# Optimization experiments

Hardware: AMD Instinct MI355X
Metric: run time of the kernel (lower is better)

Reference implementation:

```python
import jax, jax.numpy as jnp
import numpy as np

N = 100000   # nodes
E = 1600000  # edges
IN, H1, H2, OUT = 512, 64, 16, 40


def setup_inputs() -> dict:
    key = jax.random.key(0)
    ks = jax.random.split(key, 8)
    x = jax.random.normal(ks[0], (N, IN), jnp.float32)
    edge_index = jax.random.randint(ks[1], (2, E), 0, N, dtype=jnp.int64)

    def glorot(k, i, o):
        s = np.sqrt(6.0 / (i + o)).astype(np.float32)
        return jax.random.uniform(k, (i, o), jnp.float32, -s, s)

    return dict(
        x=x, edge_index=edge_index,
        W1=glorot(ks[2], IN, H1), b1=jnp.zeros((H1,), jnp.float32),
        W2=glorot(ks[3], H1, H2), b2=jnp.zeros((H2,), jnp.float32),
        W3=glorot(ks[4], H2, OUT), b3=jnp.zeros((OUT,), jnp.float32),
    )


def _gcn_conv(x, src, dst, W, b):
    # PyG GCNConv: x' = D^{-1/2} (A + I) D^{-1/2} (x W) + b
    h = x @ W                                   # [N, F_out]
    n = x.shape[0]
    deg = jnp.zeros((n,), h.dtype).at[dst].add(1.0) + 1.0   # self-loop adds 1
    dinv = jax.lax.rsqrt(deg)                   # deg >= 1 always
    norm = dinv[src] * dinv[dst]                # [E]
    msg = h[src] * norm[:, None]                # gather + scale  [E, F_out]
    out = jnp.zeros_like(h).at[dst].add(msg)    # scatter-add to targets
    out = out + h * (dinv * dinv)[:, None]      # self-loop contribution
    return out + b


def reference(x, edge_index, W1, b1, W2, b2, W3, b3):
    src, dst = edge_index[0], edge_index[1]
    h = jax.nn.relu(_gcn_conv(x, src, dst, W1, b1))
    # dropout(p=0.2, training=False) -> identity
    h = jax.nn.relu(_gcn_conv(h, src, dst, W2, b2))
    h = _gcn_conv(h, src, dst, W3, b3)
    return jax.nn.log_softmax(h, axis=-1)
```

## Files before the change

### kernel.cpp

```cpp
#include <hip/hip_runtime.h>
#include <cstdint>
#include <cstddef>

#define NNODES 100000
#define NEDGES 1600000
#define NWIN 100
#define WIN_NODES 1000
#define WCAP 17408
#define WSTR 16

#define GM_ROWS 64
#define GEMM_BLOCKS ((NNODES + GM_ROWS - 1) / GM_ROWS)
#define BUCKET_BLOCKS 512
#define BCHUNK ((NEDGES + BUCKET_BLOCKS - 1) / BUCKET_BLOCKS)
#define MEGA_BLOCKS (GEMM_BLOCKS + BUCKET_BLOCKS)

typedef __attribute__((ext_vector_type(8))) short bf16x8;
typedef __attribute__((ext_vector_type(4))) float f32x4;

__device__ inline unsigned short f2bf(float f) {
    union { float f; unsigned u; } v; v.f = f;
    unsigned r = v.u + 0x7FFFu + ((v.u >> 16) & 1u);
    return (unsigned short)(r >> 16);
}
__device__ inline void bfpair(unsigned u, float& lo, float& hi) {
    union { unsigned x; float f; } a, b;
    a.x = u << 16; b.x = u & 0xffff0000u;
    lo = a.f; hi = b.f;
}

#define GLOAD_LDS16(gp, lp)                                                        \
    __builtin_amdgcn_global_load_lds(                                              \
        (__attribute__((address_space(1))) const void*)(gp),                       \
        (__attribute__((address_space(3))) void*)(lp), 16, 0, 0)


__global__ __launch_bounds__(256) void convW(const float* __restrict__ W,
                                             unsigned short* __restrict__ Wt,
                                             int* __restrict__ wcur) {
    if (blockIdx.x == 0 && threadIdx.x < NWIN) wcur[threadIdx.x * WSTR] = 0;
    int i = blockIdx.x * 256 + threadIdx.x;
    if (i < 512 * 64) {
        int k = i >> 6, n = i & 63;
        Wt[n * 512 + k] = f2bf(W[i]);
    }
}


__global__ __launch_bounds__(256) void mega_gemm_bucket(
        const float* __restrict__ A,
        const unsigned short* __restrict__ Wt,
        unsigned short* __restrict__ Hs,
        const int* __restrict__ src, const int* __restrict__ dst,
        unsigned* __restrict__ stage,
        int* __restrict__ wcur, int M, int E) {
    __shared__ __align__(16) char smem[32768];

    long long b = blockIdx.x;
    int g0 = (int)((b * GEMM_BLOCKS) / MEGA_BLOCKS);
    int g1 = (int)(((b + 1) * GEMM_BLOCKS) / MEGA_BLOCKS);

    if (g1 > g0) {
        const int tid = threadIdx.x;
        const int wv = tid >> 6;
        const int lane = tid & 63;
        const int lm = lane & 15;
        const int lk8 = (lane >> 4);
        const int bm = g0 * GM_ROWS;
        const int wbase = bm + wv * 16;

        f32x4 acc[4];
#pragma unroll
        for (int j = 0; j < 4; j++) acc[j] = (f32x4){0.f, 0.f, 0.f, 0.f};

        const int st_rl = lane >> 4;
        const int st_u = lane & 15;

        auto ISSUE_A = [&](int k0, int bsel) {
#pragma unroll
            for (int i = 0; i < 4; i++) {
                int rl = 4 * i + st_rl;
                int grow = wbase + rl;
                grow = min(grow, M - 1);
                int su = st_u ^ rl;
                const float* gp = A + (size_t)grow * 512 + k0 + su * 4;
                char* lp = smem + bsel * 16384 + wv * 4096 + i * 1024;
                GLOAD_LDS16(gp, lp);
            }
        };

        ISSUE_A(0, 0);
        for (int t = 0; t < 8; t++) {
            const int k0 = t * 64;
            const int bsel = t & 1;

            bf16x8 bb[4][2];
#pragma unroll
            for (int cf = 0; cf < 4; cf++)
#pragma unroll
                for (int kf = 0; kf < 2; kf++)
                    bb[cf][kf] = *(const bf16x8*)&Wt[(size_t)(cf * 16 + lm) * 512
                                                     + k0 + kf * 32 + lk8 * 8];

            if (t < 7) ISSUE_A(k0 + 64, bsel ^ 1);

            if (t < 7) { asm volatile("s_waitcnt vmcnt(4)" ::: "memory"); }
            else       { asm volatile("s_waitcnt vmcnt(0)" ::: "memory"); }
            __builtin_amdgcn_sched_barrier(0);

            bf16x8 af[2];
#pragma unroll
            for (int kf = 0; kf < 2; kf++) {
                int u0 = kf * 8 + (lk8 << 1);
                const char* base = smem + bsel * 16384 + wv * 4096 + lm * 256;
                float4 lo = *(const float4*)(base + (((u0)     ^ lm) << 4));
                float4 hi = *(const float4*)(base + (((u0 + 1) ^ lm) << 4));
                unsigned c[4];
                asm("v_cvt_pk_bf16_f32 %0, %1, %2" : "=v"(c[0]) : "v"(lo.x), "v"(lo.y));
                asm("v_cvt_pk_bf16_f32 %0, %1, %2" : "=v"(c[1]) : "v"(lo.z), "v"(lo.w));
                asm("v_cvt_pk_bf16_f32 %0, %1, %2" : "=v"(c[2]) : "v"(hi.x), "v"(hi.y));
                asm("v_cvt_pk_bf16_f32 %0, %1, %2" : "=v"(c[3]) : "v"(hi.z), "v"(hi.w));
                af[kf] = *(bf16x8*)c;
            }

            __builtin_amdgcn_s_setprio(1);
#pragma unroll
            for (int kf = 0; kf < 2; kf++)
#pragma unroll
                for (int cf = 0; cf < 4; cf++)
                    acc[cf] = __builtin_amdgcn_mfma_f32_16x16x32_bf16(
                        af[kf], bb[cf][kf], acc[cf], 0, 0, 0);
            __builtin_amdgcn_s_setprio(0);
        }

#pragma unroll
        for (int j = 0; j < 4; j++) {
            int row = wbase + (lane >> 4) * 4 + j;
            if (row < M) {
#pragma unroll
                for (int cf = 0; cf < 4; cf++)
                    Hs[(size_t)row * 64 + cf * 16 + lm] = f2bf(acc[cf][j]);
            }
        }
    } else {
        int bi = (int)(b - g0);
        int* cnt  = (int*)smem;
        int* lcur = cnt + NWIN;
        const int tid = threadIdx.x;
        int e0 = bi * BCHUNK;
        int e1 = e0 + BCHUNK; if (e1 > E) e1 = E;

        for (int i = tid; i < NWIN; i += 256) cnt[i] = 0;
        __syncthreads();
        for (int e = e0 + tid; e < e1; e += 256)
            atomicAdd(&cnt[dst[e] / WIN_NODES], 1);
        __syncthreads();
        for (int i = tid; i < NWIN; i += 256)
            lcur[i] = atomicAdd(&wcur[i * WSTR], cnt[i]);
        __syncthreads();
        for (int e = e0 + tid; e < e1; e += 256) {
            int d = dst[e], s = src[e];
            int w = d / WIN_NODES;
            int pos = atomicAdd(&lcur[w], 1);
            if (pos < WCAP)
                stage[(size_t)w * WCAP + pos] =
                    ((unsigned)(d - w * WIN_NODES) << 17) | (unsigned)s;
        }
    }
}


__global__ __launch_bounds__(256) void csr_window(
        const unsigned* __restrict__ stage,
        const int* __restrict__ wcur,
        int* __restrict__ rowstart,
        float* __restrict__ dinv,
        int* __restrict__ csr) {
    __shared__ int cnt[WIN_NODES];
    __shared__ int red[256];
    const int w = blockIdx.x;
    const int t = threadIdx.x;
    const int wb = w * WIN_NODES;
    const size_t sb = (size_t)w * WCAP;

    int v = (t < w) ? min(wcur[t * WSTR], WCAP) : 0;
    red[t] = v;
    __syncthreads();
#pragma unroll
    for (int off = 128; off > 0; off >>= 1) {
        if (t < off) red[t] += red[t + off];
        __syncthreads();
    }
    int woff = red[0];
    int n_w = min(wcur[w * WSTR], WCAP);
    __syncthreads();

    for (int i = t; i < WIN_NODES; i += 256) cnt[i] = 0;
    __syncthreads();
    for (int i = t; i < n_w; i += 256)
        atomicAdd(&cnt[stage[sb + i] >> 17], 1);
    __syncthreads();

    int c0 = 0, c1 = 0, c2 = 0, c3 = 0, psum = 0;
    if (t < 250) {
        c0 = cnt[4 * t]; c1 = cnt[4 * t + 1]; c2 = cnt[4 * t + 2]; c3 = cnt[4 * t + 3];
        psum = c0 + c1 + c2 + c3;
    }
    red[t] = psum;
    __syncthreads();
#pragma unroll
    for (int off = 1; off < 256; off <<= 1) {
        int tv = (t >= off) ? red[t - off] : 0;
        __syncthreads();
        red[t] += tv;
        __syncthreads();
    }
    int excl = red[t] - psum;
    if (t < 250) {
        int running = woff + excl;
        int idx = 4 * t;
        rowstart[wb + idx] = running; dinv[wb + idx] = rsqrtf((float)c0 + 1.f);
        cnt[idx] = running; running += c0;
        rowstart[wb + idx + 1] = running; dinv[wb + idx + 1] = rsqrtf((float)c1 + 1.f);
        cnt[idx + 1] = running; running += c1;
        rowstart[wb + idx + 2] = running; dinv[wb + idx + 2] = rsqrtf((float)c2 + 1.f);
        cnt[idx + 2] = running; running += c2;
        rowstart[wb + idx + 3] = running; dinv[wb + idx + 3] = rsqrtf((float)c3 + 1.f);
        cnt[idx + 3] = running;
    }
    if (w == NWIN - 1 && t == 0) rowstart[NNODES] = woff + n_w;
    __syncthreads();

    for (int i = t; i < n_w; i += 256) {
        unsigned p = stage[sb + i];
        int dl = (int)(p >> 17);
        int s  = (int)(p & 0x1FFFFu);
        int pos = atomicAdd(&cnt[dl], 1);
        csr[pos] = s;
    }
}


__global__ __launch_bounds__(256) void gather64_l2(
        const int* __restrict__ rowstart, const int* __restrict__ csr,
        const float* __restrict__ dinv,
        const unsigned short* __restrict__ Hs1,
        const float* __restrict__ b1,
        const float* __restrict__ W2,
        unsigned short* __restrict__ Hs2,
        int M) {
    __shared__ float Ws2[64 * 16];
    __shared__ float b1s[64];
    __shared__ float srow[8][64];
    for (int i = threadIdx.x; i < 64 * 16; i += 256) Ws2[i] = W2[i];
    if (threadIdx.x < 64) b1s[threadIdx.x] = b1[threadIdx.x];
    __syncthreads();

    const int r = threadIdx.x >> 5;
    const int lf = threadIdx.x & 31;
    const int row = blockIdx.x * 8 + r;
    const bool rok = (row < M);

    float v0 = 0.f, v1 = 0.f;
    if (rok) {
        const unsigned* H32 = (const unsigned*)Hs1;
        int e0 = rowstart[row], e1 = rowstart[row + 1];
        float dd = dinv[row];
        float acc0, acc1;
        bfpair(H32[(size_t)row * 32 + lf], acc0, acc1);
        acc0 *= dd; acc1 *= dd;
        int e = e0;
        for (; e + 3 < e1; e += 4) {
            int s0 = csr[e], s1 = csr[e + 1], s2 = csr[e + 2], s3 = csr[e + 3];
            float w0 = dinv[s0], w1 = dinv[s1], w2 = dinv[s2], w3 = dinv[s3];
            unsigned u0 = H32[(size_t)s0 * 32 + lf];
            unsigned u1 = H32[(size_t)s1 * 32 + lf];
            unsigned u2 = H32[(size_t)s2 * 32 + lf];
            unsigned u3 = H32[(size_t)s3 * 32 + lf];
            float a, b;
            bfpair(u0, a, b); acc0 += w0 * a; acc1 += w0 * b;
            bfpair(u1, a, b); acc0 += w1 * a; acc1 += w1 * b;
            bfpair(u2, a, b); acc0 += w2 * a; acc1 += w2 * b;
            bfpair(u3, a, b); acc0 += w3 * a; acc1 += w3 * b;
        }
        for (; e < e1; e++) {
            int s0 = csr[e];
            float w0 = dinv[s0];
            unsigned u = H32[(size_t)s0 * 32 + lf];
            float a, b;
            bfpair(u, a, b); acc0 += w0 * a; acc1 += w0 * b;
        }
        v0 = fmaxf(acc0 * dd + b1s[2 * lf], 0.f);
        v1 = fmaxf(acc1 * dd + b1s[2 * lf + 1], 0.f);
    }
    float2 t2; t2.x = v0; t2.y = v1;
    *(float2*)&srow[r][2 * lf] = t2;
    __syncthreads();

    if (rok && lf < 16) {
        float acc = 0.f;
#pragma unroll
        for (int k4 = 0; k4 < 16; k4++) {
            float4 s4 = *(const float4*)&srow[r][k4 * 4];
            acc += s4.x * Ws2[(k4 * 4 + 0) * 16 + lf];
            acc += s4.y * Ws2[(k4 * 4 + 1) * 16 + lf];
            acc += s4.z * Ws2[(k4 * 4 + 2) * 16 + lf];
            acc += s4.w * Ws2[(k4 * 4 + 3) * 16 + lf];
        }
        acc *= dinv[row];
        float hi = __shfl_down(acc, 1, 64);
        if ((lf & 1) == 0) {
            unsigned p = (unsigned)f2bf(acc) | ((unsigned)f2bf(hi) << 16);
            ((unsigned*)Hs2)[(size_t)row * 8 + (lf >> 1)] = p;
        }
    }
}


template <int F, bool RELU, bool SCALEOUT, bool HASBIAS, bool OUTBF>
__global__ __launch_bounds__(256) void gather_bf(
        const int* __restrict__ rowstart,
        const int* __restrict__ csr,
        const float* __restrict__ dinv,
        const unsigned short* __restrict__ Hs,
        const float* __restrict__ bias,
        void* __restrict__ outp,
        int M) {
    constexpr int LANES = F / 2;
    constexpr int GP = 256 / LANES;
    int row = blockIdx.x * GP + threadIdx.x / LANES;
    int lf = threadIdx.x % LANES;
    if (row >= M) return;

    const unsigned* H32 = (const unsigned*)Hs;
    const size_t LP = F / 2;

    int e0 = rowstart[row], e1 = rowstart[row + 1];
    float acc0, acc1;
    bfpair(H32[(size_t)row * LP + lf], acc0, acc1);

    int e = e0;
    for (; e + 3 < e1; e += 4) {
        int s0 = csr[e], s1 = csr[e + 1], s2 = csr[e + 2], s3 = csr[e + 3];
        unsigned u0 = H32[(size_t)s0 * LP + lf];
        unsigned u1 = H32[(size_t)s1 * LP + lf];
        unsigned u2 = H32[(size_t)s2 * LP + lf];
        unsigned u3 = H32[(size_t)s3 * LP + lf];
        float a, b;
        bfpair(u0, a, b); acc0 += a; acc1 += b;
        bfpair(u1, a, b); acc0 += a; acc1 += b;
        bfpair(u2, a, b); acc0 += a; acc1 += b;
        bfpair(u3, a, b); acc0 += a; acc1 += b;
    }
    for (; e < e1; e++) {
        unsigned u = H32[(size_t)csr[e] * LP + lf];
        float a, b;
        bfpair(u, a, b); acc0 += a; acc1 += b;
    }

    float dd = dinv[row];
    float v0 = acc0 * dd, v1 = acc1 * dd;
    if (HASBIAS) { v0 += bias[2 * lf]; v1 += bias[2 * lf + 1]; }
    if (RELU) { v0 = fmaxf(v0, 0.f); v1 = fmaxf(v1, 0.f); }
    if (SCALEOUT) { v0 *= dd; v1 *= dd; }
    if (OUTBF) {
        unsigned p = (unsigned)f2bf(v0) | ((unsigned)f2bf(v1) << 16);
        ((unsigned*)outp)[(size_t)row * LP + lf] = p;
    } else {
        float2 t; t.x = v0; t.y = v1;
        ((float2*)outp)[(size_t)row * LP + lf] = t;
    }
}


#define SRP 20

__global__ __launch_bounds__(256) void gather16_final(
        const int* __restrict__ rowstart, const int* __restrict__ csr,
        const float* __restrict__ dinv,
        const unsigned short* __restrict__ r2s,
        const float* __restrict__ W3,
        const float* __restrict__ b3,
        float* __restrict__ out,
        int M) {
    __shared__ float Ws3[16 * 40];
    __shared__ float bs3[40];
    __shared__ float srow[32][SRP];
    __shared__ float orow[32 * 40];
    for (int i = threadIdx.x; i < 16 * 40; i += 256) Ws3[i] = W3[i];
    if (threadIdx.x < 40) bs3[threadIdx.x] = b3[threadIdx.x];

    const int r = threadIdx.x >> 3;
    const int lf = threadIdx.x & 7;
    const int row = blockIdx.x * 32 + r;
    const bool rok = (row < M);

    float g0 = 0.f, g1 = 0.f;
    if (rok) {
        const unsigned* H32 = (const unsigned*)r2s;
        int e0 = rowstart[row], e1 = rowstart[row + 1];
        float acc0, acc1;
        bfpair(H32[(size_t)row * 8 + lf], acc0, acc1);
        int e = e0;
        for (; e + 3 < e1; e += 4) {
            int s0 = csr[e], s1 = csr[e + 1], s2 = csr[e + 2], s3 = csr[e + 3];
            unsigned u0 = H32[(size_t)s0 * 8 + lf];
            unsigned u1 = H32[(size_t)s1 * 8 + lf];
            unsigned u2 = H32[(size_t)s2 * 8 + lf];
            unsigned u3 = H32[(size_t)s3 * 8 + lf];
            float a, b;
            bfpair(u0, a, b); acc0 += a; acc1 += b;
            bfpair(u1, a, b); acc0 += a; acc1 += b;
            bfpair(u2, a, b); acc0 += a; acc1 += b;
            bfpair(u3, a, b); acc0 += a; acc1 += b;
        }
        for (; e < e1; e++) {
            unsigned u = H32[(size_t)csr[e] * 8 + lf];
            float a, b;
            bfpair(u, a, b); acc0 += a; acc1 += b;
        }
        float dd = dinv[row];
        g0 = acc0 * dd; g1 = acc1 * dd;
    }
    float2 t2; t2.x = g0; t2.y = g1;
    *(float2*)&srow[r][2 * lf] = t2;
    __syncthreads();

    float vals[5];
#pragma unroll
    for (int q = 0; q < 5; q++) vals[q] = bs3[lf + 8 * q];
#pragma unroll
    for (int k4 = 0; k4 < 4; k4++) {
        float4 s4 = *(const float4*)&srow[r][k4 * 4];
#pragma unroll
        for (int q = 0; q < 5; q++) {
            int n = lf + 8 * q;
            vals[q] += s4.x * Ws3[(k4 * 4 + 0) * 40 + n];
            vals[q] += s4.y * Ws3[(k4 * 4 + 1) * 40 + n];
            vals[q] += s4.z * Ws3[(k4 * 4 + 2) * 40 + n];
            vals[q] += s4.w * Ws3[(k4 * 4 + 3) * 40 + n];
        }
    }
    float m = vals[0];
#pragma unroll
    for (int q = 1; q < 5; q++) m = fmaxf(m, vals[q]);
#pragma unroll
    for (int off = 1; off < 8; off <<= 1) m = fmaxf(m, __shfl_xor(m, off, 64));
    float s = 0.f;
#pragma unroll
    for (int q = 0; q < 5; q++) s += expf(vals[q] - m);
#pragma unroll
    for (int off = 1; off < 8; off <<= 1) s += __shfl_xor(s, off, 64);
    float ls = logf(s) + m;
#pragma unroll
    for (int q = 0; q < 5; q++) orow[r * 40 + lf + 8 * q] = vals[q] - ls;
    __syncthreads();

    float4* o4 = (float4*)(out + (size_t)blockIdx.x * 32 * 40);
    const float4* s4p = (const float4*)orow;
    for (int i = threadIdx.x; i < 320; i += 256) {
        int rr = (i * 4) / 40;
        if (blockIdx.x * 32 + rr < M) o4[i] = s4p[i];
    }
}


extern "C" void kernel_launch(void* const* d_in, const int* in_sizes, int n_in,
                              void* d_out, int out_size, void* d_ws, size_t ws_size,
                              hipStream_t stream) {
    const float* x   = (const float*)d_in[0];
    const int*   ei  = (const int*)d_in[1];
    const int*   src = ei;
    const int*   dst = ei + NEDGES;
    const float* W1 = (const float*)d_in[2];
    const float* b1 = (const float*)d_in[3];
    const float* W2 = (const float*)d_in[4];
    const float* b2 = (const float*)d_in[5];
    const float* W3 = (const float*)d_in[6];
    const float* b3 = (const float*)d_in[7];
    float* out = (float*)d_out;

    int* ws_i = (int*)d_ws;
    int* wcur     = ws_i;
    int* rowstart = wcur + NWIN * WSTR + 16;
    int* csr      = rowstart + NNODES + 8;
    unsigned* stage = (unsigned*)(csr + NEDGES);
    float* dinv   = (float*)(stage + (size_t)NWIN * WCAP);
    unsigned short* Wt = (unsigned short*)(dinv + NNODES);
    float* bufA   = (float*)((int*)(Wt + 64 * 512) + 16);
    float* bufB   = bufA + (size_t)NNODES * 64;

    unsigned short* Hs1 = (unsigned short*)bufA;
    unsigned short* Hs2 = (unsigned short*)bufB;
    unsigned short* r2s = (unsigned short*)bufA;

    convW<<<128, 256, 0, stream>>>(W1, Wt, wcur);

    mega_gemm_bucket<<<MEGA_BLOCKS, 256, 0, stream>>>(
        x, Wt, Hs1, src, dst, stage, wcur, NNODES, NEDGES);

    csr_window<<<NWIN, 256, 0, stream>>>(stage, wcur, rowstart, dinv, csr);

    gather64_l2<<<(NNODES + 7) / 8, 256, 0, stream>>>(
        rowstart, csr, dinv, Hs1, b1, W2, Hs2, NNODES);

    gather_bf<16, true, true, true, true><<<(NNODES + 31) / 32, 256, 0, stream>>>(
        rowstart, csr, dinv, Hs2, b2, r2s, NNODES);

    gather16_final<<<(NNODES + 31) / 32, 256, 0, stream>>>(
        rowstart, csr, dinv, r2s, W3, b3, out, NNODES);
}
```

Before: 226.5 us.

## Split GEMM across waves by output column with register-resident W fragments

New measurement: 210.1 us. 1.08x faster.

```diff
diff --git a/kernel.cpp b/kernel.cpp
--- a/kernel.cpp
+++ b/kernel.cpp
@@ -9,8 +9,8 @@
 #define WCAP 17408
 #define WSTR 16
 
-#define GM_ROWS 64
-#define GEMM_BLOCKS ((NNODES + GM_ROWS - 1) / GM_ROWS)
+#define GM_ROWS 16
+#define GEMM_BLOCKS (NNODES / GM_ROWS)
 #define BUCKET_BLOCKS 512
 #define BCHUNK ((NEDGES + BUCKET_BLOCKS - 1) / BUCKET_BLOCKS)
 #define MEGA_BLOCKS (GEMM_BLOCKS + BUCKET_BLOCKS)
@@ -36,25 +36,30 @@
 
 
 __global__ __launch_bounds__(256) void convW(const float* __restrict__ W,
-                                             unsigned short* __restrict__ Wt,
+                                             unsigned short* __restrict__ Wfrag,
                                              int* __restrict__ wcur) {
     if (blockIdx.x == 0 && threadIdx.x < NWIN) wcur[threadIdx.x * WSTR] = 0;
-    int i = blockIdx.x * 256 + threadIdx.x;
-    if (i < 512 * 64) {
-        int k = i >> 6, n = i & 63;
-        Wt[n * 512 + k] = f2bf(W[i]);
+    int tid = blockIdx.x * 256 + threadIdx.x;
+    if (tid < 64 * 64) {
+        int frag = tid >> 6, lane = tid & 63;
+        int cf = frag & 3, kf = (frag >> 2) & 1, t = frag >> 3;
+        int n = cf * 16 + (lane & 15);
+        int kb = t * 64 + kf * 32 + (lane >> 4) * 8;
+#pragma unroll
+        for (int j = 0; j < 8; j++)
+            Wfrag[(size_t)frag * 512 + lane * 8 + j] = f2bf(W[(size_t)(kb + j) * 64 + n]);
     }
 }
 
 
 __global__ __launch_bounds__(256) void mega_gemm_bucket(
         const float* __restrict__ A,
-        const unsigned short* __restrict__ Wt,
+        const unsigned short* __restrict__ Wfrag,
         unsigned short* __restrict__ Hs,
         const int* __restrict__ src, const int* __restrict__ dst,
         unsigned* __restrict__ stage,
         int* __restrict__ wcur, int M, int E) {
-    __shared__ __align__(16) char smem[32768];
+    __shared__ __align__(16) char smem[16384];
 
     long long b = blockIdx.x;
     int g0 = (int)((b * GEMM_BLOCKS) / MEGA_BLOCKS);
@@ -65,54 +70,49 @@
         const int wv = tid >> 6;
         const int lane = tid & 63;
         const int lm = lane & 15;
-        const int lk8 = (lane >> 4);
+        const int lk8 = lane >> 4;
         const int bm = g0 * GM_ROWS;
-        const int wbase = bm + wv * 16;
-
-        f32x4 acc[4];
-#pragma unroll
-        for (int j = 0; j < 4; j++) acc[j] = (f32x4){0.f, 0.f, 0.f, 0.f};
-
-        const int st_rl = lane >> 4;
-        const int st_u = lane & 15;
-
-        auto ISSUE_A = [&](int k0, int bsel) {
+
+        bf16x8 Breg[8][2];
+#pragma unroll
+        for (int t = 0; t < 8; t++)
+#pragma unroll
+            for (int kf = 0; kf < 2; kf++)
+                Breg[t][kf] = *(const bf16x8*)&Wfrag[(size_t)(((t * 2 + kf) * 4 + wv) * 64
+                                                              + lane) * 8];
+
+        f32x4 acc = (f32x4){0.f, 0.f, 0.f, 0.f};
+
+        auto ISSUE = [&](int t) {
+            int slot = t & 3;
 #pragma unroll
             for (int i = 0; i < 4; i++) {
-                int rl = 4 * i + st_rl;
-                int grow = wbase + rl;
-                grow = min(grow, M - 1);
-                int su = st_u ^ rl;
-                const float* gp = A + (size_t)grow * 512 + k0 + su * 4;
-                char* lp = smem + bsel * 16384 + wv * 4096 + i * 1024;
+                int rl = 4 * i + lk8;
+                int su = lm ^ rl;
+                const float* gp = A + (size_t)(bm + rl) * 512 + t * 64 + su * 4;
+                char* lp = smem + slot * 4096 + i * 1024;
                 GLOAD_LDS16(gp, lp);
             }
         };
 
-        ISSUE_A(0, 0);
+        if (wv == 0) { ISSUE(0); ISSUE(1); }
+
+#pragma unroll
         for (int t = 0; t < 8; t++) {
-            const int k0 = t * 64;
-            const int bsel = t & 1;
-
-            bf16x8 bb[4][2];
-#pragma unroll
-            for (int cf = 0; cf < 4; cf++)
-#pragma unroll
-                for (int kf = 0; kf < 2; kf++)
-                    bb[cf][kf] = *(const bf16x8*)&Wt[(size_t)(cf * 16 + lm) * 512
-                                                     + k0 + kf * 32 + lk8 * 8];
-
-            if (t < 7) ISSUE_A(k0 + 64, bsel ^ 1);
-
-            if (t < 7) { asm volatile("s_waitcnt vmcnt(4)" ::: "memory"); }
-            else       { asm volatile("s_waitcnt vmcnt(0)" ::: "memory"); }
-            __builtin_amdgcn_sched_barrier(0);
-
+            if (wv == 0) {
+                if (t + 2 < 8) ISSUE(t + 2);
+                if (t <= 5)      { asm volatile("s_waitcnt vmcnt(8)" ::: "memory"); }
+                else if (t == 6) { asm volatile("s_waitcnt vmcnt(4)" ::: "memory"); }
+                else             { asm volatile("s_waitcnt vmcnt(0)" ::: "memory"); }
+                __builtin_amdgcn_sched_barrier(0);
+            }
+            __builtin_amdgcn_s_barrier();
+
+            const char* base = smem + (t & 3) * 4096 + lm * 256;
             bf16x8 af[2];
 #pragma unroll
             for (int kf = 0; kf < 2; kf++) {
                 int u0 = kf * 8 + (lk8 << 1);
-                const char* base = smem + bsel * 16384 + wv * 4096 + lm * 256;
                 float4 lo = *(const float4*)(base + (((u0)     ^ lm) << 4));
                 float4 hi = *(const float4*)(base + (((u0 + 1) ^ lm) << 4));
                 unsigned c[4];
@@ -126,21 +126,14 @@
             __builtin_amdgcn_s_setprio(1);
 #pragma unroll
             for (int kf = 0; kf < 2; kf++)
-#pragma unroll
-                for (int cf = 0; cf < 4; cf++)
-                    acc[cf] = __builtin_amdgcn_mfma_f32_16x16x32_bf16(
-                        af[kf], bb[cf][kf], acc[cf], 0, 0, 0);
+                acc = __builtin_amdgcn_mfma_f32_16x16x32_bf16(af[kf], Breg[t][kf], acc, 0, 0, 0);
             __builtin_amdgcn_s_setprio(0);
         }
 
 #pragma unroll
         for (int j = 0; j < 4; j++) {
-            int row = wbase + (lane >> 4) * 4 + j;
-            if (row < M) {
-#pragma unroll
-                for (int cf = 0; cf < 4; cf++)
-                    Hs[(size_t)row * 64 + cf * 16 + lm] = f2bf(acc[cf][j]);
-            }
+            int row = bm + (lane >> 4) * 4 + j;
+            Hs[(size_t)row * 64 + wv * 16 + lm] = f2bf(acc[j]);
         }
     } else {
         int bi = (int)(b - g0);
@@ -486,18 +479,18 @@
     int* csr      = rowstart + NNODES + 8;
     unsigned* stage = (unsigned*)(csr + NEDGES);
     float* dinv   = (float*)(stage + (size_t)NWIN * WCAP);
-    unsigned short* Wt = (unsigned short*)(dinv + NNODES);
-    float* bufA   = (float*)((int*)(Wt + 64 * 512) + 16);
+    unsigned short* Wfrag = (unsigned short*)(dinv + NNODES);
+    float* bufA   = (float*)((int*)(Wfrag + 64 * 512) + 16);
     float* bufB   = bufA + (size_t)NNODES * 64;
 
     unsigned short* Hs1 = (unsigned short*)bufA;
     unsigned short* Hs2 = (unsigned short*)bufB;
     unsigned short* r2s = (unsigned short*)bufA;
 
-    convW<<<128, 256, 0, stream>>>(W1, Wt, wcur);
+    convW<<<16, 256, 0, stream>>>(W1, Wfrag, wcur);
 
     mega_gemm_bucket<<<MEGA_BLOCKS, 256, 0, stream>>>(
-        x, Wt, Hs1, src, dst, stage, wcur, NNODES, NEDGES);
+        x, Wfrag, Hs1, src, dst, stage, wcur, NNODES, NEDGES);
 
     csr_window<<<NWIN, 256, 0, stream>>>(stage, wcur, rowstart, dinv, csr);
 
```
